# Performance work log

Measured on AMD Instinct MI355X. Metric: run time of the kernel, lower is better.

Reference implementation:

```python
import jax, jax.numpy as jnp
import numpy as np

B, N, C, H = 8, 1024, 768, 12
D = C // H  # head_dim = 64
SCALE = D ** -0.5
EPS = 1e-5  # nn.LayerNorm default


def layer_norm(x, gamma, beta):
    # normalize over last dim (head_dim)
    mu = jnp.mean(x, axis=-1, keepdims=True)
    var = jnp.var(x, axis=-1, keepdims=True)
    return (x - mu) * jax.lax.rsqrt(var + EPS) * gamma + beta


def setup_inputs() -> dict:
    key = jax.random.key(0)
    ks = jax.random.split(key, 5)
    s = 0.02
    return {
        "x": jax.random.normal(ks[0], (B, N, C), jnp.float32),
        "qkv_w": jax.random.normal(ks[1], (3 * C, C), jnp.float32) * s,
        "qkv_b": jax.random.normal(ks[2], (3 * C,), jnp.float32) * s,
        "q_gamma": jnp.ones((D,), jnp.float32),
        "q_beta": jnp.zeros((D,), jnp.float32),
        "k_gamma": jnp.ones((D,), jnp.float32),
        "k_beta": jnp.zeros((D,), jnp.float32),
        "proj_w": jax.random.normal(ks[3], (C, C), jnp.float32) * s,
        "proj_b": jax.random.normal(ks[4], (C,), jnp.float32) * s,
    }


def reference(x, qkv_w, qkv_b, q_gamma, q_beta, k_gamma, k_beta, proj_w, proj_b):
    Bx, Nx, Cx = x.shape
    qkv = x @ qkv_w.T + qkv_b                       # [B,N,3C]
    qkv = qkv.reshape(Bx, Nx, 3, H, D).transpose(2, 0, 3, 1, 4)  # [3,B,H,N,D]
    q, k, v = qkv[0], qkv[1], qkv[2]
    q = layer_norm(q, q_gamma, q_beta) * SCALE
    k = layer_norm(k, k_gamma, k_beta)
    attn = jax.nn.softmax(jnp.einsum('bhnd,bhmd->bhnm', q, k), axis=-1)  # [B,H,N,N]
    # attn_drop is identity (p=0, eval)
    out = jnp.einsum('bhnm,bhmd->bhnd', attn, v)    # [B,H,N,D]
    out = out.transpose(0, 2, 1, 3).reshape(Bx, Nx, Cx)
    out = out @ proj_w.T + proj_b                   # proj_drop identity
    return out, attn
```

## Files before the change

### kernel.cpp

```cpp
#include <hip/hip_runtime.h>
#include <hip/hip_bf16.h>
#include <stdint.h>

typedef __bf16 bf16_t;
typedef __bf16 bf16x8 __attribute__((ext_vector_type(8)));
typedef __bf16 bf16x4 __attribute__((ext_vector_type(4)));
typedef float f32x4 __attribute__((ext_vector_type(4)));

#define DEV static __device__ __forceinline__

DEV f32x4 mfma16(bf16x8 a, bf16x8 b, f32x4 c) {
  return __builtin_amdgcn_mfma_f32_16x16x32_bf16(a, b, c, 0, 0, 0);
}

DEV void gll16(const void* g, void* l) {
  __builtin_amdgcn_global_load_lds(
      (const __attribute__((address_space(1))) uint32_t*)g,
      (__attribute__((address_space(3))) uint32_t*)l, 16, 0, 0);
}

DEV void bar_lgkm() {
  asm volatile("s_waitcnt lgkmcnt(0)" ::: "memory");
  __builtin_amdgcn_s_barrier();
  __builtin_amdgcn_sched_barrier(0);
}
#define WAIT_VM(N)                                         \
  do {                                                     \
    asm volatile("s_waitcnt vmcnt(" #N ")" ::: "memory");  \
    __builtin_amdgcn_sched_barrier(0);                     \
  } while (0)

DEV int swz128(int row, int c16) {
  return (row << 7) + (((c16 ^ row) & 7) << 4);
}
DEV int swzel128(int row, int col) {
  return (row << 7) + ((((col >> 3) ^ row) & 7) << 4) + ((col & 7) << 1);
}

DEV void stage_tile_gll(const bf16_t* g, long rstride, char* lds, int wave, int lane) {
  int r0 = wave * 8 + (lane >> 3);
  int b = lane & 7;
#pragma unroll
  for (int q = 0; q < 2; q++) {
    int row = q * 32 + r0;
    gll16(g + (long)row * rstride + (((b ^ row) & 7) << 3),
          lds + q * 4096 + wave * 1024);
  }
}

__global__ void __launch_bounds__(256)
cast_all(const float* __restrict__ x, bf16_t* __restrict__ ox,
         const float* __restrict__ w1, bf16_t* __restrict__ ow1,
         const float* __restrict__ w2, bf16_t* __restrict__ ow2) {
  long i = (long)(blockIdx.x * 256 + threadIdx.x) * 8;
  const float* s; bf16_t* d; long off;
  if (i < 6291456L)      { s = x;  d = ox;  off = i; }
  else if (i < 8060928L) { s = w1; d = ow1; off = i - 6291456L; }
  else if (i < 8650752L) { s = w2; d = ow2; off = i - 8060928L; }
  else return;
  float4 a = *(const float4*)(s + off);
  float4 b = *(const float4*)(s + off + 4);
  bf16x8 v;
  v[0] = (bf16_t)a.x; v[1] = (bf16_t)a.y; v[2] = (bf16_t)a.z; v[3] = (bf16_t)a.w;
  v[4] = (bf16_t)b.x; v[5] = (bf16_t)b.y; v[6] = (bf16_t)b.z; v[7] = (bf16_t)b.w;
  *(bf16x8*)(d + off) = v;
}

#define C1Q 0.1803368801111244f

__global__ void __launch_bounds__(256, 2)
gemm_qkv_ln(const bf16_t* __restrict__ A, const bf16_t* __restrict__ Bw,
            const float* __restrict__ bias,
            const float* __restrict__ qg, const float* __restrict__ qb,
            const float* __restrict__ kg, const float* __restrict__ kb,
            bf16_t* __restrict__ qkv, int M, int N, int K) {
  __shared__ __align__(16) char As[8192];
  __shared__ __align__(16) char Bs[8192];
  const int tid = threadIdx.x;
  const int lane = tid & 63;
  const int wave = tid >> 6;
  const int wr = wave >> 1, wc = wave & 1;
  const int tileM = blockIdx.y << 7;
  const int tileN = blockIdx.x << 7;
  const int lrow = lane & 15, lk = lane >> 4;

  f32x4 acc[4][4];
  f32x4 z = {0.f, 0.f, 0.f, 0.f};
#pragma unroll
  for (int m = 0; m < 4; m++)
#pragma unroll
    for (int n = 0; n < 4; n++) acc[m][n] = z;

  const int srow = wave * 16 + (lane >> 2);
  const int sb = lane & 3;
  const bf16_t* Asrc0 = A + (long)(tileM + srow) * K + sb * 8;
  const bf16_t* Asrc1 = A + (long)(tileM + 64 + srow) * K + sb * 8;
  const bf16_t* Bsrc0 = Bw + (long)(tileN + srow) * K + sb * 8;
  const bf16_t* Bsrc1 = Bw + (long)(tileN + 64 + srow) * K + sb * 8;
  char* Adst = As + wave * 1024;
  char* Bdst = Bs + wave * 1024;

  for (int k0 = 0; k0 < K; k0 += 32) {
    __syncthreads();
    gll16(Asrc0 + k0, Adst);
    gll16(Asrc1 + k0, Adst + 4096);
    gll16(Bsrc0 + k0, Bdst);
    gll16(Bsrc1 + k0, Bdst + 4096);
    __syncthreads();
    bf16x8 af[4], bfr[4];
#pragma unroll
    for (int m = 0; m < 4; m++)
      af[m] = *(const bf16x8*)(As + (wr * 64 + m * 16 + lrow) * 64 + lk * 16);
#pragma unroll
    for (int n = 0; n < 4; n++)
      bfr[n] = *(const bf16x8*)(Bs + (wc * 64 + n * 16 + lrow) * 64 + lk * 16);
#pragma unroll
    for (int m = 0; m < 4; m++)
#pragma unroll
      for (int n = 0; n < 4; n++)
        acc[m][n] = mfma16(af[m], bfr[n], acc[m][n]);
  }

  const int t = tileN / 768;
  const int cbase = tileN + wc * 64;
  float g[4], be[4], bv[4];
#pragma unroll
  for (int n = 0; n < 4; n++) bv[n] = bias[cbase + n * 16 + lrow];
  if (t == 0) {
#pragma unroll
    for (int n = 0; n < 4; n++) {
      int d = n * 16 + lrow;
      g[n] = qg[d] * C1Q; be[n] = qb[d] * C1Q;
    }
  } else if (t == 1) {
#pragma unroll
    for (int n = 0; n < 4; n++) {
      int d = n * 16 + lrow;
      g[n] = kg[d]; be[n] = kb[d];
    }
  }

#pragma unroll
  for (int m = 0; m < 4; m++) {
#pragma unroll
    for (int r = 0; r < 4; r++) {
      float v[4];
#pragma unroll
      for (int n = 0; n < 4; n++) v[n] = acc[m][n][r] + bv[n];
      long row = tileM + wr * 64 + m * 16 + lk * 4 + r;
      bf16_t* dst = qkv + row * 2304 + cbase;
      if (t < 2) {
        float s = v[0] + v[1] + v[2] + v[3];
        float s2 = v[0]*v[0] + v[1]*v[1] + v[2]*v[2] + v[3]*v[3];
#pragma unroll
        for (int ofs = 1; ofs <= 8; ofs <<= 1) {
          s  += __shfl_xor(s, ofs);
          s2 += __shfl_xor(s2, ofs);
        }
        float mu = s * (1.f / 64.f);
        float rstd = rsqrtf(s2 * (1.f / 64.f) - mu * mu + 1e-5f);
#pragma unroll
        for (int n = 0; n < 4; n++)
          dst[n * 16 + lrow] = (bf16_t)((v[n] - mu) * rstd * g[n] + be[n]);
      } else {
#pragma unroll
        for (int n = 0; n < 4; n++)
          dst[n * 16 + lrow] = (bf16_t)v[n];
      }
    }
  }
}

__global__ void __launch_bounds__(256, 2)
gemm_bt(const bf16_t* __restrict__ A, const bf16_t* __restrict__ Bw,
        const float* __restrict__ bias, float* __restrict__ Cout,
        int M, int N, int K) {
  __shared__ __align__(16) char As[8192];
  __shared__ __align__(16) char Bs[8192];
  const int tid = threadIdx.x;
  const int lane = tid & 63;
  const int wave = tid >> 6;
  const int wr = wave >> 1, wc = wave & 1;
  const int tileM = blockIdx.y << 7;
  const int tileN = blockIdx.x << 7;
  const int lrow = lane & 15, lk = lane >> 4;

  f32x4 acc[4][4];
  f32x4 z = {0.f, 0.f, 0.f, 0.f};
#pragma unroll
  for (int m = 0; m < 4; m++)
#pragma unroll
    for (int n = 0; n < 4; n++) acc[m][n] = z;

  const int srow = wave * 16 + (lane >> 2);
  const int sb = lane & 3;
  const bf16_t* Asrc0 = A + (long)(tileM + srow) * K + sb * 8;
  const bf16_t* Asrc1 = A + (long)(tileM + 64 + srow) * K + sb * 8;
  const bf16_t* Bsrc0 = Bw + (long)(tileN + srow) * K + sb * 8;
  const bf16_t* Bsrc1 = Bw + (long)(tileN + 64 + srow) * K + sb * 8;
  char* Adst = As + wave * 1024;
  char* Bdst = Bs + wave * 1024;

  for (int k0 = 0; k0 < K; k0 += 32) {
    __syncthreads();
    gll16(Asrc0 + k0, Adst);
    gll16(Asrc1 + k0, Adst + 4096);
    gll16(Bsrc0 + k0, Bdst);
    gll16(Bsrc1 + k0, Bdst + 4096);
    __syncthreads();
    bf16x8 af[4], bfr[4];
#pragma unroll
    for (int m = 0; m < 4; m++)
      af[m] = *(const bf16x8*)(As + (wr * 64 + m * 16 + lrow) * 64 + lk * 16);
#pragma unroll
    for (int n = 0; n < 4; n++)
      bfr[n] = *(const bf16x8*)(Bs + (wc * 64 + n * 16 + lrow) * 64 + lk * 16);
#pragma unroll
    for (int m = 0; m < 4; m++)
#pragma unroll
      for (int n = 0; n < 4; n++)
        acc[m][n] = mfma16(af[m], bfr[n], acc[m][n]);
  }

  const int rg = lk;
#pragma unroll
  for (int n = 0; n < 4; n++) {
    int col = tileN + wc * 64 + n * 16 + lrow;
    float bv = bias[col];
#pragma unroll
    for (int m = 0; m < 4; m++) {
      long row0 = tileM + wr * 64 + m * 16 + rg * 4;
#pragma unroll
      for (int r = 0; r < 4; r++)
        Cout[(row0 + r) * N + col] = acc[m][n][r] + bv;
    }
  }
}

__global__ void __launch_bounds__(256, 2)
attn_kernel(const bf16_t* __restrict__ qkv, float* __restrict__ attn_out,
            bf16_t* __restrict__ out_heads) {
  const int tid = threadIdx.x;
  const int lane = tid & 63;
  const int wave = tid >> 6;
  const int qt = blockIdx.x;
  const int bh = blockIdx.y;
  const int b = bh / 12, h = bh - b * 12;

  const bf16_t* base = qkv + (long)b * 2359296L + h * 64;
  const bf16_t* Qg = base;
  const bf16_t* Kg = base + 768;
  const bf16_t* Vg = base + 1536;

  __shared__ __align__(16) char Ks[16384];
  __shared__ __align__(16) char Vt[8192];
  __shared__ __align__(16) char QP[8192];

  const int lrow = lane & 15;
  const int lk = lane >> 4;

  stage_tile_gll(Qg + (long)(qt * 64) * 2304, 2304, QP, wave, lane);
  stage_tile_gll(Kg, 2304, Ks, wave, lane);
  __syncthreads();

  bf16x8 qf[2];
  qf[0] = *(const bf16x8*)(QP + swz128(wave * 16 + lrow, lk));
  qf[1] = *(const bf16x8*)(QP + swz128(wave * 16 + lrow, 4 + lk));

  auto computeS = [&](const char* Kb, f32x4 sfr[4]) {
    f32x4 z = {0.f, 0.f, 0.f, 0.f};
    sfr[0] = z; sfr[1] = z; sfr[2] = z; sfr[3] = z;
#pragma unroll
    for (int kk = 0; kk < 2; kk++)
#pragma unroll
      for (int f = 0; f < 4; f++) {
        bf16x8 kf = *(const bf16x8*)(Kb + swz128(f * 16 + lrow, kk * 4 + lk));
        sfr[f] = mfma16(qf[kk], kf, sfr[f]);
      }
  };

  float l_r[4] = {0.f, 0.f, 0.f, 0.f};

  for (int kt = 0; kt < 16; kt++) {
    if (kt < 15) {
      stage_tile_gll(Kg + (long)((kt + 1) * 64) * 2304, 2304,
                     Ks + ((kt + 1) & 1) * 8192, wave, lane);
      __builtin_amdgcn_sched_barrier(0);
      WAIT_VM(2);
    } else {
      WAIT_VM(0);
    }
    f32x4 sfr[4];
    computeS(Ks + (kt & 1) * 8192, sfr);
#pragma unroll
    for (int r = 0; r < 4; r++)
      l_r[r] += exp2f(sfr[0][r]) + exp2f(sfr[1][r]) +
                exp2f(sfr[2][r]) + exp2f(sfr[3][r]);
    bar_lgkm();
  }

  float il[4];
#pragma unroll
  for (int r = 0; r < 4; r++) {
#pragma unroll
    for (int ofs = 1; ofs <= 8; ofs <<= 1)
      l_r[r] += __shfl_xor(l_r[r], ofs);
    il[r] = 1.0f / l_r[r];
  }

  f32x4 of[4];
  {
    f32x4 z = {0.f, 0.f, 0.f, 0.f};
    of[0] = z; of[1] = z; of[2] = z; of[3] = z;
  }
  char* Pw = QP + wave * 2048;
  float* attn_base = attn_out + (long)bh * 1048576 + ((long)(qt * 64) << 10);

  stage_tile_gll(Kg, 2304, Ks, wave, lane);
  const int vk = lane, vdg = wave;
  bf16x8 vr0 = *(const bf16x8*)(Vg + (long)vk * 2304 + vdg * 16);
  bf16x8 vr1 = *(const bf16x8*)(Vg + (long)vk * 2304 + vdg * 16 + 8);
  WAIT_VM(0);

  for (int kt = 0; kt < 16; kt++) {
    bar_lgkm();
    WAIT_VM(4);
#pragma unroll
    for (int j = 0; j < 8; j++) {
      *(bf16_t*)(Vt + swzel128(vdg * 16 + j, vk)) = vr0[j];
      *(bf16_t*)(Vt + swzel128(vdg * 16 + 8 + j, vk)) = vr1[j];
    }
    f32x4 sfr[4];
    computeS(Ks + (kt & 1) * 8192, sfr);
#pragma unroll
    for (int f = 0; f < 4; f++)
#pragma unroll
      for (int r = 0; r < 4; r++) {
        float p = exp2f(sfr[f][r]) * il[r];
        *(bf16_t*)(Pw + swzel128(lk * 4 + r, f * 16 + lrow)) = (bf16_t)p;
      }
    bar_lgkm();
    if (kt < 15) {
      stage_tile_gll(Kg + (long)((kt + 1) * 64) * 2304, 2304,
                     Ks + ((kt + 1) & 1) * 8192, wave, lane);
      const bf16_t* vp = Vg + (long)((kt + 1) * 64 + vk) * 2304 + vdg * 16;
      vr0 = *(const bf16x8*)(vp);
      vr1 = *(const bf16x8*)(vp + 8);
      __builtin_amdgcn_sched_barrier(0);
    }
#pragma unroll
    for (int kk = 0; kk < 2; kk++) {
      bf16x8 pf = *(const bf16x8*)(Pw + swz128(lrow, kk * 4 + lk));
#pragma unroll
      for (int f = 0; f < 4; f++) {
        bf16x8 vf = *(const bf16x8*)(Vt + swz128(f * 16 + lrow, kk * 4 + lk));
        of[f] = mfma16(pf, vf, of[f]);
      }
    }
    float* ab = attn_base + kt * 64;
    {
      const int rsub = lane >> 4;
      const int c8 = lane & 15;
      const char* psrc = Pw + (c8 & 1) * 8;
#pragma unroll
      for (int i = 0; i < 4; i++) {
        int rl = i * 4 + rsub;
        bf16x4 pv = *(const bf16x4*)(psrc + swz128(rl, c8 >> 1));
        f32x4 v = {(float)pv[0], (float)pv[1], (float)pv[2], (float)pv[3]};
        __builtin_nontemporal_store(
            v, (f32x4*)(ab + ((long)(wave * 16 + rl) << 10) + c8 * 4));
      }
    }
  }

#pragma unroll
  for (int f = 0; f < 4; f++)
#pragma unroll
    for (int r = 0; r < 4; r++) {
      int nrow = qt * 64 + wave * 16 + lk * 4 + r;
      int d = f * 16 + lrow;
      out_heads[((long)b * 1024 + nrow) * 768 + h * 64 + d] = (bf16_t)of[f][r];
    }
}

extern "C" void kernel_launch(void* const* d_in, const int* in_sizes, int n_in,
                              void* d_out, int out_size, void* d_ws, size_t ws_size,
                              hipStream_t stream) {
  (void)in_sizes; (void)n_in; (void)out_size; (void)ws_size;
  const float* x       = (const float*)d_in[0];
  const float* qkv_w   = (const float*)d_in[1];
  const float* qkv_b   = (const float*)d_in[2];
  const float* q_gamma = (const float*)d_in[3];
  const float* q_beta  = (const float*)d_in[4];
  const float* k_gamma = (const float*)d_in[5];
  const float* k_beta  = (const float*)d_in[6];
  const float* proj_w  = (const float*)d_in[7];
  const float* proj_b  = (const float*)d_in[8];
  float* out = (float*)d_out;

  char* ws = (char*)d_ws;
  bf16_t* x_bf      = (bf16_t*)(ws);
  bf16_t* wqkv      = (bf16_t*)(ws + 12582912L);
  bf16_t* wproj     = (bf16_t*)(ws + 16121856L);
  bf16_t* qkv       = (bf16_t*)(ws + 17301504L);
  bf16_t* out_heads = (bf16_t*)(ws + 55050240L);

  cast_all<<<4224, 256, 0, stream>>>(x, x_bf, qkv_w, wqkv, proj_w, wproj);
  gemm_qkv_ln<<<dim3(18, 64), 256, 0, stream>>>(x_bf, wqkv, qkv_b,
                                                q_gamma, q_beta, k_gamma, k_beta,
                                                qkv, 8192, 2304, 768);
  attn_kernel<<<dim3(16, 96), 256, 0, stream>>>(qkv, out + 6291456L, out_heads);
  gemm_bt<<<dim3(6, 64), 256, 0, stream>>>(out_heads, wproj, proj_b, out, 8192, 768, 768);
}
```

Baseline: 211.4 us.

## Remap block IDs to XCD-contiguous tiles and defer vmcnt waits in attention

```diff
diff --git a/kernel.cpp b/kernel.cpp
--- a/kernel.cpp
+++ b/kernel.cpp
@@ -80,8 +80,10 @@
   const int lane = tid & 63;
   const int wave = tid >> 6;
   const int wr = wave >> 1, wc = wave & 1;
-  const int tileM = blockIdx.y << 7;
-  const int tileN = blockIdx.x << 7;
+  const int lb = blockIdx.x;
+  const int sid = (lb & 7) * 144 + (lb >> 3);
+  const int tileM = (sid / 18) << 7;
+  const int tileN = (sid % 18) << 7;
   const int lrow = lane & 15, lk = lane >> 4;
 
   f32x4 acc[4][4];
@@ -181,8 +183,10 @@
   const int lane = tid & 63;
   const int wave = tid >> 6;
   const int wr = wave >> 1, wc = wave & 1;
-  const int tileM = blockIdx.y << 7;
-  const int tileN = blockIdx.x << 7;
+  const int lb = blockIdx.x;
+  const int sid = (lb & 7) * 48 + (lb >> 3);
+  const int tileM = (sid / 6) << 7;
+  const int tileN = (sid % 6) << 7;
   const int lrow = lane & 15, lk = lane >> 4;
 
   f32x4 acc[4][4];
@@ -243,8 +247,10 @@
   const int tid = threadIdx.x;
   const int lane = tid & 63;
   const int wave = tid >> 6;
-  const int qt = blockIdx.x;
-  const int bh = blockIdx.y;
+  const int lb = blockIdx.x;
+  const int sid = (lb & 7) * 192 + (lb >> 3);
+  const int qt = sid & 15;
+  const int bh = sid >> 4;
   const int b = bh / 12, h = bh - b * 12;
 
   const bf16_t* base = qkv + (long)b * 2359296L + h * 64;
@@ -286,9 +292,6 @@
       stage_tile_gll(Kg + (long)((kt + 1) * 64) * 2304, 2304,
                      Ks + ((kt + 1) & 1) * 8192, wave, lane);
       __builtin_amdgcn_sched_barrier(0);
-      WAIT_VM(2);
-    } else {
-      WAIT_VM(0);
     }
     f32x4 sfr[4];
     computeS(Ks + (kt & 1) * 8192, sfr);
@@ -296,6 +299,7 @@
     for (int r = 0; r < 4; r++)
       l_r[r] += exp2f(sfr[0][r]) + exp2f(sfr[1][r]) +
                 exp2f(sfr[2][r]) + exp2f(sfr[3][r]);
+    if (kt < 15) WAIT_VM(0);
     bar_lgkm();
   }
 
@@ -324,7 +328,6 @@
 
   for (int kt = 0; kt < 16; kt++) {
     bar_lgkm();
-    WAIT_VM(4);
 #pragma unroll
     for (int j = 0; j < 8; j++) {
       *(bf16_t*)(Vt + swzel128(vdg * 16 + j, vk)) = vr0[j];
@@ -371,6 +374,7 @@
             v, (f32x4*)(ab + ((long)(wave * 16 + rl) << 10) + c8 * 4));
       }
     }
+    if (kt < 15) WAIT_VM(6);
   }
 
 #pragma unroll
@@ -406,9 +410,9 @@
   bf16_t* out_heads = (bf16_t*)(ws + 55050240L);
 
   cast_all<<<4224, 256, 0, stream>>>(x, x_bf, qkv_w, wqkv, proj_w, wproj);
-  gemm_qkv_ln<<<dim3(18, 64), 256, 0, stream>>>(x_bf, wqkv, qkv_b,
-                                                q_gamma, q_beta, k_gamma, k_beta,
-                                                qkv, 8192, 2304, 768);
-  attn_kernel<<<dim3(16, 96), 256, 0, stream>>>(qkv, out + 6291456L, out_heads);
-  gemm_bt<<<dim3(6, 64), 256, 0, stream>>>(out_heads, wproj, proj_b, out, 8192, 768, 768);
-}
+  gemm_qkv_ln<<<1152, 256, 0, stream>>>(x_bf, wqkv, qkv_b,
+                                        q_gamma, q_beta, k_gamma, k_beta,
+                                        qkv, 8192, 2304, 768);
+  attn_kernel<<<1536, 256, 0, stream>>>(qkv, out + 6291456L, out_heads);
+  gemm_bt<<<384, 256, 0, stream>>>(out_heads, wproj, proj_b, out, 8192, 768, 768);
+}
```

Result: faster. 193.4 us (-8.5%).
